# Kernel tuning notes

Hardware: AMD Instinct MI355X
Metric: run time of the kernel (lower is better)

The kernel has to match this reference:

```python
import jax, jax.numpy as jnp
import numpy as np

GROUP_SIZE = 128  # cfg.group_size

def dequantize_int4(weight_q, scale, zero_point, group_size):
    # weight_q: (out, in) int values in [0,15]; scale/zero_point: (out, n_groups)
    out_f, in_f = weight_q.shape
    n_groups = in_f // group_size
    w = weight_q.astype(jnp.float32).reshape(out_f, n_groups, group_size)
    w = (w - zero_point[:, :, None]) * scale[:, :, None]
    return w.reshape(out_f, in_f)

def setup_inputs() -> dict:
    key = jax.random.key(0)
    k1, k2, k3, k4, k5 = jax.random.split(key, 5)
    B, S, D_IN, D_OUT = 2, 2048, 4096, 4096
    n_groups = D_IN // GROUP_SIZE
    x = jax.random.normal(k1, (B, S, D_IN), dtype=jnp.float32)
    weight_q = jax.random.randint(k2, (D_OUT, D_IN), 0, 16, dtype=jnp.int32)
    scale = jax.random.uniform(k3, (D_OUT, n_groups), dtype=jnp.float32, minval=0.001, maxval=0.02)
    zero_point = jax.random.uniform(k4, (D_OUT, n_groups), dtype=jnp.float32, minval=0.0, maxval=15.0)
    bias = jax.random.normal(k5, (D_OUT,), dtype=jnp.float32)
    return {"x": x, "weight_q": weight_q, "scale": scale, "zero_point": zero_point, "bias": bias}

def reference(x, weight_q, scale, zero_point, bias):
    # Faithful to QuantizedLinear.forward with bits=4: dequantize then F.linear
    w = dequantize_int4(weight_q, scale, zero_point, GROUP_SIZE).astype(x.dtype)  # (out, in)
    return jnp.einsum('bsi,oi->bso', x, w) + bias
```

## Files before the change

kernel.cpp:

```cpp
#include <hip/hip_runtime.h>

typedef __bf16 bf16x8 __attribute__((ext_vector_type(8)));
typedef float f32x4 __attribute__((ext_vector_type(4)));

__device__ __forceinline__ void gload16(const void* g, void* l) {
    __builtin_amdgcn_global_load_lds(
        (const __attribute__((address_space(1))) unsigned int*)g,
        (__attribute__((address_space(3))) unsigned int*)l, 16, 0, 0);
}

__global__ void k_prep(const float* __restrict__ x, __bf16* __restrict__ xb, size_t nx,
                       const int* __restrict__ wq, const float* __restrict__ scale,
                       const float* __restrict__ zp, __bf16* __restrict__ wb,
                       int K, int GS, int NG, int nxb) {
    const int bid = (int)blockIdx.x;
    if (bid < nxb) {
        size_t i = ((size_t)bid * blockDim.x + threadIdx.x) * 8;
        if (i >= nx) return;
        const float4 a = *(const float4*)(x + i);
        const float4 b = *(const float4*)(x + i + 4);
        bf16x8 v;
        v[0] = (__bf16)a.x; v[1] = (__bf16)a.y; v[2] = (__bf16)a.z; v[3] = (__bf16)a.w;
        v[4] = (__bf16)b.x; v[5] = (__bf16)b.y; v[6] = (__bf16)b.z; v[7] = (__bf16)b.w;
        *(bf16x8*)(xb + i) = v;
    } else {
        size_t i = ((size_t)(bid - nxb) * blockDim.x + threadIdx.x) * 8;
        int o = (int)(i / K);
        int k = (int)(i % K);
        int g = k / GS;
        float s = scale[(size_t)o * NG + g];
        float z = zp[(size_t)o * NG + g];
        const int4 q0 = *(const int4*)(wq + i);
        const int4 q1 = *(const int4*)(wq + i + 4);
        bf16x8 v;
        v[0] = (__bf16)(((float)q0.x - z) * s); v[1] = (__bf16)(((float)q0.y - z) * s);
        v[2] = (__bf16)(((float)q0.z - z) * s); v[3] = (__bf16)(((float)q0.w - z) * s);
        v[4] = (__bf16)(((float)q1.x - z) * s); v[5] = (__bf16)(((float)q1.y - z) * s);
        v[6] = (__bf16)(((float)q1.z - z) * s); v[7] = (__bf16)(((float)q1.w - z) * s);
        *(bf16x8*)(wb + i) = v;
    }
}

__global__ void k_dequant_w(const int* __restrict__ wq, const float* __restrict__ scale,
                            const float* __restrict__ zp, __bf16* __restrict__ wb,
                            int K, int GS, int NG) {
    size_t i = ((size_t)blockIdx.x * blockDim.x + threadIdx.x) * 8;
    int o = (int)(i / K);
    int k = (int)(i % K);
    int g = k / GS;
    float s = scale[(size_t)o * NG + g];
    float z = zp[(size_t)o * NG + g];
    const int4 q0 = *(const int4*)(wq + i);
    const int4 q1 = *(const int4*)(wq + i + 4);
    bf16x8 v;
    v[0] = (__bf16)(((float)q0.x - z) * s); v[1] = (__bf16)(((float)q0.y - z) * s);
    v[2] = (__bf16)(((float)q0.z - z) * s); v[3] = (__bf16)(((float)q0.w - z) * s);
    v[4] = (__bf16)(((float)q1.x - z) * s); v[5] = (__bf16)(((float)q1.y - z) * s);
    v[6] = (__bf16)(((float)q1.z - z) * s); v[7] = (__bf16)(((float)q1.w - z) * s);
    *(bf16x8*)(wb + i) = v;
}

#define BKg 32
#define TILEB 32768
#define ATILEB 16384

__global__ __launch_bounds__(512, 2) void k_gemm256(
    const __bf16* __restrict__ A, const __bf16* __restrict__ B,
    const float* __restrict__ bias, float* __restrict__ C,
    int M, int N, int K)
{
    __shared__ __align__(16) char lds[4 * TILEB];
    const int tid = threadIdx.x;
    const int w = tid >> 6, lane = tid & 63;
    const int wm = w >> 2, wn = w & 3;
    const int lr = lane & 15, hi = lane >> 4;
    const int NT = K / BKg;

    const int nbx = N / 256;
    const int nwg = nbx * (M / 256);
    const int bid = (int)blockIdx.x;
    const int q = nwg >> 3, r = nwg & 7;
    const int xcd = bid & 7, loc = bid >> 3;
    const int swz = (xcd < r ? xcd * (q + 1) : r * (q + 1) + (xcd - r) * q) + loc;
    const int m0 = (swz / nbx) * 256;
    const int n0 = (swz % nbx) * 256;

    size_t aOff[2], bOff[2];
#pragma unroll
    for (int L = 0; L < 2; ++L) {
        int c = L * 512 + tid;
        int row = c >> 2, ch = (c & 3) ^ ((c >> 3) & 3);
        aOff[L] = (size_t)(m0 + row) * K + ch * 8;
        bOff[L] = (size_t)(n0 + row) * K + ch * 8;
    }
    int dstOff[2];
#pragma unroll
    for (int L = 0; L < 2; ++L) dstOff[L] = (L * 512 + w * 64) * 16;

    const int chR = (hi ^ ((lr >> 1) & 3)) * 16;
    const int aRd = (wm * 128 + lr) * 64 + chR;
    const int bRd = ATILEB + (wn * 64 + lr) * 64 + chR;

#define STAGE_A(tt, buf) do {                                              \
    const int kk_ = (tt) * BKg;                                            \
    gload16(A + aOff[0] + kk_, lds + (buf) * TILEB + dstOff[0]);           \
    gload16(A + aOff[1] + kk_, lds + (buf) * TILEB + dstOff[1]);           \
} while (0)
#define STAGE_B(tt, buf) do {                                              \
    const int kk_ = (tt) * BKg;                                            \
    gload16(B + bOff[0] + kk_, lds + (buf) * TILEB + ATILEB + dstOff[0]);  \
    gload16(B + bOff[1] + kk_, lds + (buf) * TILEB + ATILEB + dstOff[1]);  \
} while (0)
#define RD_A(dst, buf, m) dst = *(const bf16x8*)(lds + (buf) * TILEB + aRd + (m) * 1024)
#define RD_B(dst, buf, n) dst = *(const bf16x8*)(lds + (buf) * TILEB + bRd + (n) * 1024)

    f32x4 acc[8][4] = {};
    bf16x8 a03[4], a47[4], b0[4], b1[4];

    STAGE_A(0, 0); STAGE_B(0, 0);
    STAGE_A(1, 1); STAGE_B(1, 1);
    STAGE_A(2, 2); STAGE_B(2, 2);
    asm volatile("s_waitcnt vmcnt(8)" ::: "memory");
    __builtin_amdgcn_s_barrier();
    RD_A(a03[0], 0, 0); RD_A(a03[1], 0, 1); RD_A(a03[2], 0, 2); RD_A(a03[3], 0, 3);
    RD_B(b0[0], 0, 0);  RD_B(b0[1], 0, 1);  RD_B(b0[2], 0, 2);  RD_B(b0[3], 0, 3);

#define ITER(t, BCUR, BNXT) do {                                            \
    const int bt = (t) & 3, bt1 = ((t) + 1) & 3, bt3 = ((t) + 3) & 3;       \
    int t3 = (t) + 3; if (t3 >= NT) t3 -= NT;                               \
                      \
    asm volatile("s_waitcnt vmcnt(4)" ::: "memory");                        \
    __builtin_amdgcn_s_barrier();                                           \
                \
    STAGE_A(t3, bt3);                                                       \
    RD_A(a47[0], bt, 4); RD_A(a47[1], bt, 5);                               \
    RD_A(a47[2], bt, 6); RD_A(a47[3], bt, 7);                               \
    asm volatile("s_waitcnt lgkmcnt(4)" ::: "memory");                      \
    __builtin_amdgcn_sched_barrier(0);                                      \
    __builtin_amdgcn_s_setprio(1);                                          \
    _Pragma("unroll")                                                       \
    for (int m_ = 0; m_ < 4; ++m_)                                          \
        _Pragma("unroll")                                                   \
        for (int n_ = 0; n_ < 4; ++n_)                                      \
            acc[m_][n_] = __builtin_amdgcn_mfma_f32_16x16x32_bf16(          \
                a03[m_], BCUR[n_], acc[m_][n_], 0, 0, 0);                   \
    __builtin_amdgcn_s_setprio(0);                                          \
    __builtin_amdgcn_sched_barrier(0);                                      \
            \
    STAGE_B(t3, bt3);                                                       \
    if ((t) + 1 < NT) {                                                     \
        RD_A(a03[0], bt1, 0); RD_A(a03[1], bt1, 1);                         \
        RD_A(a03[2], bt1, 2); RD_A(a03[3], bt1, 3);                         \
        RD_B(BNXT[0], bt1, 0); RD_B(BNXT[1], bt1, 1);                       \
        RD_B(BNXT[2], bt1, 2); RD_B(BNXT[3], bt1, 3);                       \
        asm volatile("s_waitcnt lgkmcnt(8)" ::: "memory");                  \
    } else {                                                                \
        asm volatile("s_waitcnt lgkmcnt(0)" ::: "memory");                  \
    }                                                                       \
    __builtin_amdgcn_sched_barrier(0);                                      \
    __builtin_amdgcn_s_setprio(1);                                          \
    _Pragma("unroll")                                                       \
    for (int m_ = 0; m_ < 4; ++m_)                                          \
        _Pragma("unroll")                                                   \
        for (int n_ = 0; n_ < 4; ++n_)                                      \
            acc[m_ + 4][n_] = __builtin_amdgcn_mfma_f32_16x16x32_bf16(      \
                a47[m_], BCUR[n_], acc[m_ + 4][n_], 0, 0, 0);               \
    __builtin_amdgcn_s_setprio(0);                                          \
    __builtin_amdgcn_sched_barrier(0);                                      \
} while (0)

    for (int t = 0; t < NT; t += 2) {
        ITER(t,     b0, b1);
        ITER(t + 1, b1, b0);
    }

    asm volatile("s_waitcnt vmcnt(0)" ::: "memory");

#pragma unroll
    for (int n_ = 0; n_ < 4; ++n_) {
        const int col = n0 + wn * 64 + n_ * 16 + lr;
        const float bv = bias[col];
#pragma unroll
        for (int m_ = 0; m_ < 8; ++m_) {
            const size_t rbase = (size_t)(m0 + wm * 128 + m_ * 16 + hi * 4) * N + col;
            C[rbase]                 = acc[m_][n_][0] + bv;
            C[rbase + N]             = acc[m_][n_][1] + bv;
            C[rbase + 2 * (size_t)N] = acc[m_][n_][2] + bv;
            C[rbase + 3 * (size_t)N] = acc[m_][n_][3] + bv;
        }
    }
#undef ITER
#undef STAGE_A
#undef STAGE_B
#undef RD_A
#undef RD_B
}

template <int MODE>
__global__ __launch_bounds__(256, 2) void k_gemm(
    const __bf16* __restrict__ Ab, const float* __restrict__ Af,
    const __bf16* __restrict__ Bb, const int* __restrict__ Bq,
    const float* __restrict__ scale, const float* __restrict__ zp,
    const float* __restrict__ bias, float* __restrict__ C,
    int M, int N, int K, int NG, int GS)
{
    __shared__ __align__(16) __bf16 As[128 * 32];
    __shared__ __align__(16) __bf16 Bs[128 * 32];

    const int tid  = threadIdx.x;
    const int w    = tid >> 6;
    const int lane = tid & 63;
    const int wm   = w >> 1, wn = w & 1;
    const int m0   = blockIdx.y * 128, n0 = blockIdx.x * 128;
    const int lr   = lane & 15;
    const int lc   = lane >> 4;

    f32x4 acc[4][4] = {};

    for (int kk = 0; kk < K; kk += 32) {
        if constexpr (MODE == 0) {
#pragma unroll
            for (int i = 0; i < 2; i++) {
                int c = i * 256 + tid;
                const __bf16* g = Ab + (size_t)(m0 + (c >> 2)) * K + kk + (c & 3) * 8;
                gload16(g, (char*)As + (i * 256 + w * 64) * 16);
            }
        } else {
            int row = tid >> 1, half = tid & 1;
            const float* g = Af + (size_t)(m0 + row) * K + kk + half * 16;
            float4 f0 = *(const float4*)g;
            float4 f1 = *(const float4*)(g + 4);
            float4 f2 = *(const float4*)(g + 8);
            float4 f3 = *(const float4*)(g + 12);
            bf16x8 v0, v1;
            v0[0] = (__bf16)f0.x; v0[1] = (__bf16)f0.y; v0[2] = (__bf16)f0.z; v0[3] = (__bf16)f0.w;
            v0[4] = (__bf16)f1.x; v0[5] = (__bf16)f1.y; v0[6] = (__bf16)f1.z; v0[7] = (__bf16)f1.w;
            v1[0] = (__bf16)f2.x; v1[1] = (__bf16)f2.y; v1[2] = (__bf16)f2.z; v1[3] = (__bf16)f2.w;
            v1[4] = (__bf16)f3.x; v1[5] = (__bf16)f3.y; v1[6] = (__bf16)f3.z; v1[7] = (__bf16)f3.w;
            *(bf16x8*)(As + row * 32 + half * 16)     = v0;
            *(bf16x8*)(As + row * 32 + half * 16 + 8) = v1;
        }
        if constexpr (MODE <= 1) {
#pragma unroll
            for (int i = 0; i < 2; i++) {
                int c = i * 256 + tid;
                const __bf16* g = Bb + (size_t)(n0 + (c >> 2)) * K + kk + (c & 3) * 8;
                gload16(g, (char*)Bs + (i * 256 + w * 64) * 16);
            }
        } else {
            int row = tid >> 1, half = tid & 1;
            int o = n0 + row;
            int kbase = kk + half * 16;
            int g = kbase / GS;
            float s = scale[(size_t)o * NG + g];
            float z = zp[(size_t)o * NG + g];
            const int* qp = Bq + (size_t)o * K + kbase;
            int4 q0 = *(const int4*)qp;
            int4 q1 = *(const int4*)(qp + 4);
            int4 q2 = *(const int4*)(qp + 8);
            int4 q3 = *(const int4*)(qp + 12);
            bf16x8 v0, v1;
            v0[0] = (__bf16)(((float)q0.x - z) * s); v0[1] = (__bf16)(((float)q0.y - z) * s);
            v0[2] = (__bf16)(((float)q0.z - z) * s); v0[3] = (__bf16)(((float)q0.w - z) * s);
            v0[4] = (__bf16)(((float)q1.x - z) * s); v0[5] = (__bf16)(((float)q1.y - z) * s);
            v0[6] = (__bf16)(((float)q1.z - z) * s); v0[7] = (__bf16)(((float)q1.w - z) * s);
            v1[0] = (__bf16)(((float)q2.x - z) * s); v1[1] = (__bf16)(((float)q2.y - z) * s);
            v1[2] = (__bf16)(((float)q2.z - z) * s); v1[3] = (__bf16)(((float)q2.w - z) * s);
            v1[4] = (__bf16)(((float)q3.x - z) * s); v1[5] = (__bf16)(((float)q3.y - z) * s);
            v1[6] = (__bf16)(((float)q3.z - z) * s); v1[7] = (__bf16)(((float)q3.w - z) * s);
            *(bf16x8*)(Bs + row * 32 + half * 16)     = v0;
            *(bf16x8*)(Bs + row * 32 + half * 16 + 8) = v1;
        }

        __syncthreads();

        bf16x8 af[4], bfm[4];
#pragma unroll
        for (int a = 0; a < 4; a++)
            af[a] = *(const bf16x8*)(As + (wm * 64 + a * 16 + lr) * 32 + lc * 8);
#pragma unroll
        for (int b = 0; b < 4; b++)
            bfm[b] = *(const bf16x8*)(Bs + (wn * 64 + b * 16 + lr) * 32 + lc * 8);
#pragma unroll
        for (int a = 0; a < 4; a++)
#pragma unroll
            for (int b = 0; b < 4; b++)
                acc[a][b] = __builtin_amdgcn_mfma_f32_16x16x32_bf16(af[a], bfm[b], acc[a][b], 0, 0, 0);

        __syncthreads();
    }

#pragma unroll
    for (int b = 0; b < 4; b++) {
        int col = n0 + wn * 64 + b * 16 + lr;
        float bv = bias[col];
#pragma unroll
        for (int a = 0; a < 4; a++) {
            int rbase = m0 + wm * 64 + a * 16 + lc * 4;
#pragma unroll
            for (int r = 0; r < 4; r++)
                C[(size_t)(rbase + r) * N + col] = acc[a][b][r] + bv;
        }
    }
}

extern "C" void kernel_launch(void* const* d_in, const int* in_sizes, int n_in,
                              void* d_out, int out_size, void* d_ws, size_t ws_size,
                              hipStream_t stream) {
    const float* x     = (const float*)d_in[0];
    const int*   wq    = (const int*)d_in[1];
    const float* scale = (const float*)d_in[2];
    const float* zp    = (const float*)d_in[3];
    const float* bias  = (const float*)d_in[4];
    float* out = (float*)d_out;

    const int    N  = in_sizes[4];
    const long   K  = in_sizes[1] / N;
    const long   M  = in_sizes[0] / K;
    const int    NG = in_sizes[2] / N;
    const int    GS = (int)(K / NG);

    const size_t wbytes = (size_t)N * K * sizeof(__bf16);
    const size_t xbytes = (size_t)M * K * sizeof(__bf16);

    char* ws = (char*)d_ws;
    __bf16* wb = (__bf16*)ws;
    __bf16* xb = (__bf16*)(ws + wbytes);

    const bool big = (M % 256 == 0) && (N % 256 == 0) && (K % 64 == 0) && (K / 32 >= 4);

    if (ws_size >= wbytes + xbytes) {
        size_t nx = (size_t)M * K;
        size_t nw = (size_t)N * K;
        unsigned nxb = (unsigned)((nx / 8 + 255) / 256);
        unsigned nwb = (unsigned)((nw / 8 + 255) / 256);
        k_prep<<<nxb + nwb, 256, 0, stream>>>(x, xb, nx, wq, scale, zp, wb,
                                              (int)K, GS, NG, (int)nxb);
        if (big) {
            unsigned nwg = (unsigned)((M / 256) * (N / 256));
            k_gemm256<<<nwg, 512, 0, stream>>>(xb, wb, bias, out, (int)M, N, (int)K);
        } else {
            dim3 grid((unsigned)(N / 128), (unsigned)(M / 128)), blk(256);
            k_gemm<0><<<grid, blk, 0, stream>>>(xb, nullptr, wb, nullptr, scale, zp, bias, out,
                                                (int)M, N, (int)K, NG, GS);
        }
    } else if (ws_size >= wbytes) {
        size_t nw = (size_t)N * K;
        dim3 grid((unsigned)(N / 128), (unsigned)(M / 128)), blk(256);
        k_dequant_w<<<(unsigned)((nw / 8 + 255) / 256), 256, 0, stream>>>(wq, scale, zp, wb, (int)K, GS, NG);
        k_gemm<1><<<grid, blk, 0, stream>>>(nullptr, x, wb, nullptr, scale, zp, bias, out,
                                            (int)M, N, (int)K, NG, GS);
    } else {
        dim3 grid((unsigned)(N / 128), (unsigned)(M / 128)), blk(256);
        k_gemm<2><<<grid, blk, 0, stream>>>(nullptr, x, nullptr, wq, scale, zp, bias, out,
                                            (int)M, N, (int)K, NG, GS);
    }
}
```

Before: 144.6 us.

## Restructure 256x256 GEMM pipeline to BK=64 double buffer with phased staging

Changes the main GEMM's K-tile from 32 to 64 and replaces the 4-deep ring of 32-wide buffers with two 64-wide buffers, each split into two k-subslices. The loop now runs eight compute phases per pair of tiles, and each phase issues one slice of global-to-LDS loads, waits, synchronises with barriers and then runs 16 MFMAs. The aim is fewer pipeline iterations and finer interleaving of loads with compute. In exchange it adds a barrier before and after every phase, drains all LDS reads with lgkmcnt(0) instead of keeping register prefetch, and tightens the eligibility check to K divisible by 128.

```diff
diff --git a/kernel.cpp b/kernel.cpp
--- a/kernel.cpp
+++ b/kernel.cpp
@@ -60,16 +60,15 @@
     *(bf16x8*)(wb + i) = v;
 }
 
-#define BKg 32
-#define TILEB 32768
-#define ATILEB 16384
+#define BKg 64
+#define BUFB 65536
 
 __global__ __launch_bounds__(512, 2) void k_gemm256(
     const __bf16* __restrict__ A, const __bf16* __restrict__ B,
     const float* __restrict__ bias, float* __restrict__ C,
     int M, int N, int K)
 {
-    __shared__ __align__(16) char lds[4 * TILEB];
+    __shared__ __align__(16) char lds[2 * BUFB];
     const int tid = threadIdx.x;
     const int w = tid >> 6, lane = tid & 63;
     const int wm = w >> 2, wn = w & 3;
@@ -99,82 +98,88 @@
 
     const int chR = (hi ^ ((lr >> 1) & 3)) * 16;
     const int aRd = (wm * 128 + lr) * 64 + chR;
-    const int bRd = ATILEB + (wn * 64 + lr) * 64 + chR;
-
-#define STAGE_A(tt, buf) do {                                              \
-    const int kk_ = (tt) * BKg;                                            \
-    gload16(A + aOff[0] + kk_, lds + (buf) * TILEB + dstOff[0]);           \
-    gload16(A + aOff[1] + kk_, lds + (buf) * TILEB + dstOff[1]);           \
+    const int bRd = 32768 + (wn * 64 + lr) * 64 + chR;
+
+#define STG_A(tt, BUF, KS) do {                                            \
+    gload16(A + aOff[0] + (tt) * BKg + (KS) * 32,                          \
+            lds + (BUF) * BUFB + (KS) * 16384 + dstOff[0]);                \
+    gload16(A + aOff[1] + (tt) * BKg + (KS) * 32,                          \
+            lds + (BUF) * BUFB + (KS) * 16384 + dstOff[1]);                \
 } while (0)
-#define STAGE_B(tt, buf) do {                                              \
-    const int kk_ = (tt) * BKg;                                            \
-    gload16(B + bOff[0] + kk_, lds + (buf) * TILEB + ATILEB + dstOff[0]);  \
-    gload16(B + bOff[1] + kk_, lds + (buf) * TILEB + ATILEB + dstOff[1]);  \
+#define STG_B(tt, BUF, KS) do {                                            \
+    gload16(B + bOff[0] + (tt) * BKg + (KS) * 32,                          \
+            lds + (BUF) * BUFB + 32768 + (KS) * 16384 + dstOff[0]);        \
+    gload16(B + bOff[1] + (tt) * BKg + (KS) * 32,                          \
+            lds + (BUF) * BUFB + 32768 + (KS) * 16384 + dstOff[1]);        \
 } while (0)
-#define RD_A(dst, buf, m) dst = *(const bf16x8*)(lds + (buf) * TILEB + aRd + (m) * 1024)
-#define RD_B(dst, buf, n) dst = *(const bf16x8*)(lds + (buf) * TILEB + bRd + (n) * 1024)
+#define RD_A(dst, BUF, KS, m) \
+    dst = *(const bf16x8*)(lds + (BUF) * BUFB + (KS) * 16384 + aRd + (m) * 1024)
+#define RD_B(dst, BUF, KS, n) \
+    dst = *(const bf16x8*)(lds + (BUF) * BUFB + (KS) * 16384 + bRd + (n) * 1024)
+#define VMW(n) asm volatile("s_waitcnt vmcnt(" #n ")" ::: "memory")
 
     f32x4 acc[8][4] = {};
-    bf16x8 a03[4], a47[4], b0[4], b1[4];
-
-    STAGE_A(0, 0); STAGE_B(0, 0);
-    STAGE_A(1, 1); STAGE_B(1, 1);
-    STAGE_A(2, 2); STAGE_B(2, 2);
-    asm volatile("s_waitcnt vmcnt(8)" ::: "memory");
+    bf16x8 a03[4], a47[4], bfr[4];
+
+#define PH03(BUF, KS, STG, VM) do {                                          \
+    RD_A(a03[0], BUF, KS, 0); RD_A(a03[1], BUF, KS, 1);                      \
+    RD_A(a03[2], BUF, KS, 2); RD_A(a03[3], BUF, KS, 3);                      \
+    RD_B(bfr[0], BUF, KS, 0); RD_B(bfr[1], BUF, KS, 1);                      \
+    RD_B(bfr[2], BUF, KS, 2); RD_B(bfr[3], BUF, KS, 3);                      \
+    STG;                                                                     \
+    VM;                                                                      \
+    __builtin_amdgcn_s_barrier();                                            \
+    asm volatile("s_waitcnt lgkmcnt(0)" ::: "memory");                       \
+    __builtin_amdgcn_sched_barrier(0);                                       \
+    __builtin_amdgcn_s_setprio(1);                                           \
+    _Pragma("unroll")                                                        \
+    for (int m_ = 0; m_ < 4; ++m_)                                           \
+        _Pragma("unroll")                                                    \
+        for (int n_ = 0; n_ < 4; ++n_)                                       \
+            acc[m_][n_] = __builtin_amdgcn_mfma_f32_16x16x32_bf16(           \
+                a03[m_], bfr[n_], acc[m_][n_], 0, 0, 0);                     \
+    __builtin_amdgcn_s_setprio(0);                                           \
+    __builtin_amdgcn_s_barrier();                                            \
+} while (0)
+
+#define PH47(BUF, KS, STG, VM) do {                                          \
+    RD_A(a47[0], BUF, KS, 4); RD_A(a47[1], BUF, KS, 5);                      \
+    RD_A(a47[2], BUF, KS, 6); RD_A(a47[3], BUF, KS, 7);                      \
+    STG;                                                                     \
+    VM;                                                                      \
+    __builtin_amdgcn_s_barrier();                                            \
+    asm volatile("s_waitcnt lgkmcnt(0)" ::: "memory");                       \
+    __builtin_amdgcn_sched_barrier(0);                                       \
+    __builtin_amdgcn_s_setprio(1);                                           \
+    _Pragma("unroll")                                                        \
+    for (int m_ = 0; m_ < 4; ++m_)                                           \
+        _Pragma("unroll")                                                    \
+        for (int n_ = 0; n_ < 4; ++n_)                                       \
+            acc[m_ + 4][n_] = __builtin_amdgcn_mfma_f32_16x16x32_bf16(       \
+                a47[m_], bfr[n_], acc[m_ + 4][n_], 0, 0, 0);                 \
+    __builtin_amdgcn_s_setprio(0);                                           \
+    __builtin_amdgcn_s_barrier();                                            \
+} while (0)
+
+    STG_A(0, 0, 0); STG_A(0, 0, 1); STG_B(0, 0, 0); STG_B(0, 0, 1);
+    STG_B(1, 1, 0); STG_A(1, 1, 0); STG_B(1, 1, 1);
+    VMW(6);
     __builtin_amdgcn_s_barrier();
-    RD_A(a03[0], 0, 0); RD_A(a03[1], 0, 1); RD_A(a03[2], 0, 2); RD_A(a03[3], 0, 3);
-    RD_B(b0[0], 0, 0);  RD_B(b0[1], 0, 1);  RD_B(b0[2], 0, 2);  RD_B(b0[3], 0, 3);
-
-#define ITER(t, BCUR, BNXT) do {                                            \
-    const int bt = (t) & 3, bt1 = ((t) + 1) & 3, bt3 = ((t) + 3) & 3;       \
-    int t3 = (t) + 3; if (t3 >= NT) t3 -= NT;                               \
-                      \
-    asm volatile("s_waitcnt vmcnt(4)" ::: "memory");                        \
-    __builtin_amdgcn_s_barrier();                                           \
-                \
-    STAGE_A(t3, bt3);                                                       \
-    RD_A(a47[0], bt, 4); RD_A(a47[1], bt, 5);                               \
-    RD_A(a47[2], bt, 6); RD_A(a47[3], bt, 7);                               \
-    asm volatile("s_waitcnt lgkmcnt(4)" ::: "memory");                      \
-    __builtin_amdgcn_sched_barrier(0);                                      \
-    __builtin_amdgcn_s_setprio(1);                                          \
-    _Pragma("unroll")                                                       \
-    for (int m_ = 0; m_ < 4; ++m_)                                          \
-        _Pragma("unroll")                                                   \
-        for (int n_ = 0; n_ < 4; ++n_)                                      \
-            acc[m_][n_] = __builtin_amdgcn_mfma_f32_16x16x32_bf16(          \
-                a03[m_], BCUR[n_], acc[m_][n_], 0, 0, 0);                   \
-    __builtin_amdgcn_s_setprio(0);                                          \
-    __builtin_amdgcn_sched_barrier(0);                                      \
-            \
-    STAGE_B(t3, bt3);                                                       \
-    if ((t) + 1 < NT) {                                                     \
-        RD_A(a03[0], bt1, 0); RD_A(a03[1], bt1, 1);                         \
-        RD_A(a03[2], bt1, 2); RD_A(a03[3], bt1, 3);                         \
-        RD_B(BNXT[0], bt1, 0); RD_B(BNXT[1], bt1, 1);                       \
-        RD_B(BNXT[2], bt1, 2); RD_B(BNXT[3], bt1, 3);                       \
-        asm volatile("s_waitcnt lgkmcnt(8)" ::: "memory");                  \
-    } else {                                                                \
-        asm volatile("s_waitcnt lgkmcnt(0)" ::: "memory");                  \
-    }                                                                       \
-    __builtin_amdgcn_sched_barrier(0);                                      \
-    __builtin_amdgcn_s_setprio(1);                                          \
-    _Pragma("unroll")                                                       \
-    for (int m_ = 0; m_ < 4; ++m_)                                          \
-        _Pragma("unroll")                                                   \
-        for (int n_ = 0; n_ < 4; ++n_)                                      \
-            acc[m_ + 4][n_] = __builtin_amdgcn_mfma_f32_16x16x32_bf16(      \
-                a47[m_], BCUR[n_], acc[m_ + 4][n_], 0, 0, 0);               \
-    __builtin_amdgcn_s_setprio(0);                                          \
-    __builtin_amdgcn_sched_barrier(0);                                      \
-} while (0)
 
     for (int t = 0; t < NT; t += 2) {
-        ITER(t,     b0, b1);
-        ITER(t + 1, b1, b0);
-    }
-
-    asm volatile("s_waitcnt vmcnt(0)" ::: "memory");
+        int t2 = t + 2; if (t2 >= NT) t2 -= NT;
+        int t3 = t + 3; if (t3 >= NT) t3 -= NT;
+        PH03(0, 0, STG_A(t + 1, 1, 1), (void)0);
+        PH47(0, 0, STG_B(t2, 0, 0),    (void)0);
+        PH03(0, 1, STG_A(t2, 0, 0),    (void)0);
+        PH47(0, 1, STG_B(t2, 0, 1),    VMW(6));
+        PH03(1, 0, STG_A(t2, 0, 1),    (void)0);
+        PH47(1, 0, STG_B(t3, 1, 0),    (void)0);
+        PH03(1, 1, STG_A(t3, 1, 0),    (void)0);
+        PH47(1, 1, STG_B(t3, 1, 1),    VMW(6));
+    }
+
+    VMW(0);
 
 #pragma unroll
     for (int n_ = 0; n_ < 4; ++n_) {
@@ -189,11 +194,13 @@
             C[rbase + 3 * (size_t)N] = acc[m_][n_][3] + bv;
         }
     }
-#undef ITER
-#undef STAGE_A
-#undef STAGE_B
+#undef PH03
+#undef PH47
+#undef STG_A
+#undef STG_B
 #undef RD_A
 #undef RD_B
+#undef VMW
 }
 
 template <int MODE>
@@ -327,7 +334,7 @@
     __bf16* wb = (__bf16*)ws;
     __bf16* xb = (__bf16*)(ws + wbytes);
 
-    const bool big = (M % 256 == 0) && (N % 256 == 0) && (K % 64 == 0) && (K / 32 >= 4);
+    const bool big = (M % 256 == 0) && (N % 256 == 0) && (K % 128 == 0) && (K / 64 >= 4);
 
     if (ws_size >= wbytes + xbytes) {
         size_t nx = (size_t)M * K;
```

Result: slower. 151.4 us (+4.7%).
